# Performance work log

Hardware: AMD Instinct MI355X
Metric: run time of the kernel (lower is better)

Reference implementation:

```python
import jax, jax.numpy as jnp
import numpy as np
from jax import lax

T = 8192; BLK = 32; M = 64; C = 32; D = 512; HH = 256; L = 6; TEMP = 1.0

def _gru(x, Wih, Whh, bih, bhh, reverse=False):
    # x: (S, B, in) -> (S, B, h); PyTorch GRU cell math
    h0 = jnp.zeros((x.shape[1], Whh.shape[0]), x.dtype)
    xs = x[::-1] if reverse else x
    gi = xs @ Wih + bih
    def step(h, g):
        gh = h @ Whh + bhh
        ir, iz, inn = jnp.split(g, 3, -1)
        hr, hz, hn = jnp.split(gh, 3, -1)
        r = jax.nn.sigmoid(ir + hr)
        z = jax.nn.sigmoid(iz + hz)
        n = jnp.tanh(inn + r * hn)
        h = (1.0 - z) * n + z * h
        return h, h
    _, hs = lax.scan(step, h0, gi)
    return hs[::-1] if reverse else hs

def _xattn(X, Y, Xpos, Ypos, Wq, Wk, Wv, Wo, bo):
    # Y queries X; single head with head_dim = D (X2Y_map)
    q = (Y + Ypos) @ Wq
    k = (X + Xpos) @ Wk
    v = X @ Wv
    logits = jnp.einsum('ybd,xbd->byx', q, k) / jnp.sqrt(jnp.float32(q.shape[-1]))
    attn = jax.nn.softmax(logits, -1)
    out = jnp.einsum('byx,xbd->ybd', attn, v) @ Wo + bo
    return out, attn, logits

def _conv1(x, W, b, dil=1):
    y = lax.conv_general_dilated(x, W, (1,), 'SAME', rhs_dilation=(dil,), dimension_numbers=('NCH', 'OIH', 'NCH'))
    return y + b[None, :, None]

def _sim(x, W, b, text):
    v = x @ W + b
    v = v / jnp.linalg.norm(v, axis=-1, keepdims=True)
    t = text / jnp.linalg.norm(text, axis=-1, keepdims=True)
    return jnp.einsum('tbh,ch->tbc', v, t) / TEMP

def _segments(frame_feature, Wf2c, bf2c, text):
    # host-side argmax -> contiguous-run segmentation (mirrors utils.parse_label on CPU)
    sim = _sim(frame_feature, Wf2c, bf2c, text)
    pred = np.asarray(jnp.argmax(sim[:, 0], -1))
    change = np.concatenate([[0], (np.diff(pred) != 0).astype(np.int64)])
    seg_id = np.cumsum(change)
    S = int(seg_id[-1]) + 1
    starts = np.concatenate([[0], np.flatnonzero(change)])
    ends = np.concatenate([starts[1:] - 1, [len(pred) - 1]])
    centers = (starts + ends) // 2
    return jnp.asarray(seg_id), S, jnp.asarray(centers)

def _core(p, seg_id, S, centers):
    ff = p['frame_feature']
    cnt = jax.ops.segment_sum(jnp.ones((T,), jnp.float32), seg_id, S)
    seg = jax.ops.segment_sum(ff, seg_id, S) / cnt[:, None, None]  # frame->seg mean pool
    hf = _gru(seg, p['sg_Wih_f'], p['sg_Whh_f'], p['sg_bih_f'], p['sg_bhh_f'])
    hb = _gru(seg, p['sg_Wih_b'], p['sg_Whh_b'], p['sg_bih_b'], p['sg_bhh_b'], reverse=True)
    seg = jax.nn.relu(jnp.concatenate([hf, hb], -1)) @ p['Wcomb'] + p['bcomb']
    seg_pos = p['frame_pos'][centers]
    af, _, _ = _xattn(seg, p['action_feature'], seg_pos, p['action_pos'], p['f2a_Wq'], p['f2a_Wk'], p['f2a_Wv'], p['f2a_Wo'], p['f2a_bo'])
    af = _gru(af, p['ag_Wih'], p['ag_Whh'], p['ag_bih'], p['ag_bhh'])  # action branch GRU
    seg2, _, _ = _xattn(af, seg, p['action_pos'], seg_pos, p['a2f_Wq'], p['a2f_Wk'], p['a2f_Wv'], p['a2f_Wo'], p['a2f_bo'])
    s2f = seg2[seg_id]  # seg->frame upsample
    ff2 = jax.nn.relu(jnp.concatenate([s2f, ff], -1) @ p['Wsf'] + p['bsf'])
    x = jnp.transpose(ff2[:, 0])[None]  # (1, D, T)
    x = _conv1(x, p['tcn_in_W'], p['tcn_in_b'])
    for i in range(L):  # dilated residual TCN (MSTCN)
        y = jax.nn.relu(_conv1(x, p['tcn_dW'][i], p['tcn_db'][i], dil=2 ** i))
        x = x + _conv1(y, p['tcn_pW'][i], p['tcn_pb'][i])
    x = _conv1(x, p['tcn_out_W'], p['tcn_out_b'])
    ff_out = jnp.transpose(x[0])[:, None, :]
    return ff_out, af, seg2

def setup_inputs():
    ks = iter(jax.random.split(jax.random.key(0), 80))
    def rn(*shape):
        return jax.random.normal(next(ks), shape, dtype=jnp.float32)
    def z(n):
        return jnp.zeros((n,), jnp.float32)
    s = 0.05
    base = rn(T // BLK, 1, D)
    frame_feature = jnp.repeat(base, BLK, axis=0) + 0.01 * rn(T, 1, D)
    return {
        'frame_feature': frame_feature,
        'action_feature': rn(M, 1, D),
        'frame_pos': 0.02 * rn(T, 1, D),
        'action_pos': 0.02 * rn(M, 1, D),
        'text_emb': rn(C, 512),
        'Wf2c': s * rn(D, 512), 'bf2c': z(512),
        'Wa2c': s * rn(D, 512), 'ba2c': z(512),
        'Ws2c': s * rn(D, 512), 'bs2c': z(512),
        'sg_Wih_f': s * rn(D, 3 * HH), 'sg_Whh_f': s * rn(HH, 3 * HH), 'sg_bih_f': z(3 * HH), 'sg_bhh_f': z(3 * HH),
        'sg_Wih_b': s * rn(D, 3 * HH), 'sg_Whh_b': s * rn(HH, 3 * HH), 'sg_bih_b': z(3 * HH), 'sg_bhh_b': z(3 * HH),
        'Wcomb': s * rn(D, D), 'bcomb': z(D),
        'f2a_Wq': s * rn(D, D), 'f2a_Wk': s * rn(D, D), 'f2a_Wv': s * rn(D, D), 'f2a_Wo': s * rn(D, D), 'f2a_bo': z(D),
        'ag_Wih': s * rn(D, 3 * D), 'ag_Whh': s * rn(D, 3 * D), 'ag_bih': z(3 * D), 'ag_bhh': z(3 * D),
        'a2f_Wq': s * rn(D, D), 'a2f_Wk': s * rn(D, D), 'a2f_Wv': s * rn(D, D), 'a2f_Wo': s * rn(D, D), 'a2f_bo': z(D),
        'Wsf': s * rn(2 * D, D), 'bsf': z(D),
        'tcn_in_W': s * rn(D, D, 1), 'tcn_in_b': z(D),
        'tcn_dW': s * rn(L, D, D, 3), 'tcn_db': jnp.zeros((L, D), jnp.float32),
        'tcn_pW': s * rn(L, D, D, 1), 'tcn_pb': jnp.zeros((L, D), jnp.float32),
        'tcn_out_W': s * rn(D, D, 1), 'tcn_out_b': z(D),
    }

def reference(frame_feature, action_feature, frame_pos, action_pos, text_emb, Wf2c, bf2c, Wa2c, ba2c, Ws2c, bs2c, sg_Wih_f, sg_Whh_f, sg_bih_f, sg_bhh_f, sg_Wih_b, sg_Whh_b, sg_bih_b, sg_bhh_b, Wcomb, bcomb, f2a_Wq, f2a_Wk, f2a_Wv, f2a_Wo, f2a_bo, ag_Wih, ag_Whh, ag_bih, ag_bhh, a2f_Wq, a2f_Wk, a2f_Wv, a2f_Wo, a2f_bo, Wsf, bsf, tcn_in_W, tcn_in_b, tcn_dW, tcn_db, tcn_pW, tcn_pb, tcn_out_W, tcn_out_b):
    p = dict(locals())
    seg_id, S, centers = _segments(frame_feature, Wf2c, bf2c, text_emb)
    ff_out, af, seg2 = _core(p, seg_id, S, centers)
    frame_sim = _sim(ff_out, Wf2c, bf2c, text_emb)
    action_sim = _sim(af, Wa2c, ba2c, text_emb)
    seg_sim = _sim(seg2, Ws2c, bs2c, text_emb)
    return ff_out, af, frame_sim, action_sim, seg_sim
```

## Files before the change

kernel.cpp:

```cpp
#include <hip/hip_runtime.h>
#include <cstdint>
#include <cstddef>

__device__ __forceinline__ float sigf(float x) { return 1.f / (1.f + expf(-x)); }

__device__ __forceinline__ unsigned packh(float a, float b) {
  union { unsigned u; _Float16 h[2]; } cv;
  cv.h[0] = (_Float16)a; cv.h[1] = (_Float16)b; return cv.u;
}
__device__ __forceinline__ float2 uph(unsigned u) {
  union { unsigned uu; _Float16 h[2]; } cv; cv.uu = u;
  return make_float2((float)cv.h[0], (float)cv.h[1]);
}

typedef _Float16 f16x8 __attribute__((ext_vector_type(8)));
typedef float f32x16 __attribute__((ext_vector_type(16)));

static constexpr int TT = 8192;
static constexpr int MM = 64;
static constexpr int CC = 32;
static constexpr int DD = 512;
static constexpr unsigned GUARD_MAX = 1u << 30;

__global__ void zero_k(float* __restrict__ p, long n) {
  long i = (long)blockIdx.x * 256 + threadIdx.x;
  long stride = (long)gridDim.x * 256;
  for (; i < n; i += stride) p[i] = 0.f;
}

__global__ void copy_k(const float* __restrict__ a, float* __restrict__ o, int n) {
  int i = blockIdx.x * 256 + threadIdx.x;
  if (i < n) o[i] = a[i];
}
__global__ void addff_k(const float* __restrict__ a, const float* __restrict__ b, float* __restrict__ o, int n) {
  int i = blockIdx.x * 256 + threadIdx.x;
  if (i < n) o[i] = a[i] + b[i];
}
__global__ void acomb_k(const float* __restrict__ hf, const float* __restrict__ hb, float* __restrict__ o, int n) {
  int i = blockIdx.x * 256 + threadIdx.x;
  if (i >= n) return;
  int s = i >> 9, j = i & 511;
  float v = (j < 256) ? hf[(size_t)s * 256 + j] : hb[(size_t)s * 256 + (j - 256)];
  o[i] = fmaxf(v, 0.f);
}
__global__ void gatherpos_k(const float* __restrict__ fpos, const int* __restrict__ centers,
                            float* __restrict__ segpos, int n) {
  int i = blockIdx.x * 256 + threadIdx.x;
  if (i >= n) return;
  int s = i >> 9, dd = i & 511;
  int ct = centers[s];
  ct = ct < 0 ? 0 : (ct > TT - 1 ? TT - 1 : ct);
  segpos[i] = fpos[(size_t)ct * 512 + dd];
}

__global__ void tnorm_k(const float* __restrict__ text, float* __restrict__ tnorm) {
  int c = blockIdx.x * 256 + threadIdx.x;
  if (c >= 32) return;
  float s = 0.f;
  for (int dd = 0; dd < 512; dd++) { float v = text[(size_t)c * 512 + dd]; s += v * v; }
  tnorm[c] = sqrtf(s);
}

__global__ void prepM_k(const float* __restrict__ W, const float* __restrict__ b,
                        const float* __restrict__ text, const float* __restrict__ tnorm,
                        float* __restrict__ M, float* __restrict__ bdot) {
  int idx = blockIdx.x * 256 + threadIdx.x;
  if (idx < 512 * 32) {
    int k = idx >> 5, c = idx & 31;
    const float* wr = W + (size_t)k * 512;
    const float* tr = text + (size_t)c * 512;
    float s = 0.f;
    for (int dd = 0; dd < 512; dd++) s += wr[dd] * tr[dd];
    M[idx] = s / tnorm[c];
  }
  if (idx < 32) {
    const float* tr = text + (size_t)idx * 512;
    float s = 0.f;
    for (int dd = 0; dd < 512; dd++) s += b[dd] * tr[dd];
    bdot[idx] = s / tnorm[idx];
  }
}

__launch_bounds__(256)
__global__ void fargmax_k(const float* __restrict__ ff, const float* __restrict__ M,
                          const float* __restrict__ bdot, int* __restrict__ pred) {
  const int r = blockIdx.x * 8 + (threadIdx.x >> 5);
  const int c = threadIdx.x & 31;
  const float* fr = ff + (size_t)r * 512;
  float acc = bdot[c];
  for (int k = 0; k < 512; k++) acc += fr[k] * M[k * 32 + c];
  float best = acc; int bidx = c;
  for (int off = 16; off >= 1; off >>= 1) {
    const float ov = __shfl_xor(best, off);
    const int oi = __shfl_xor(bidx, off);
    if (ov > best || (ov == best && oi < bidx)) { best = ov; bidx = oi; }
  }
  if (c == 0) pred[r] = bidx;
}

__global__ void nlogit_k(const float* __restrict__ Q, const float* __restrict__ Kk,
                         float* __restrict__ L, int NY, int NX) {
  int idx = blockIdx.x * 256 + threadIdx.x;
  if (idx >= NY * NX) return;
  int y = idx / NX, x = idx - y * NX;
  const float* qr = Q + (size_t)y * 512;
  const float* kr = Kk + (size_t)x * 512;
  float d = 0.f;
  for (int k = 0; k < 512; k++) d += qr[k] * kr[k];
  L[idx] = d * 0.044194173824159216f;
}
__global__ void nsoft_k(float* __restrict__ L, int NY, int NX) {
  int y = blockIdx.x * 256 + threadIdx.x;
  if (y >= NY) return;
  float* row = L + (size_t)y * NX;
  float m = row[0];
  for (int x = 1; x < NX; x++) m = fmaxf(m, row[x]);
  float s = 0.f;
  for (int x = 0; x < NX; x++) { float p = expf(row[x] - m); row[x] = p; s += p; }
  const float inv = 1.f / s;
  for (int x = 0; x < NX; x++) row[x] *= inv;
}
__global__ void nav_k(const float* __restrict__ P, const float* __restrict__ V,
                      float* __restrict__ O, int NY, int NX) {
  int idx = blockIdx.x * 256 + threadIdx.x;
  if (idx >= NY * 512) return;
  int y = idx >> 9, dd = idx & 511;
  const float* pr = P + (size_t)y * NX;
  float o = 0.f;
  for (int x = 0; x < NX; x++) o += pr[x] * V[(size_t)x * 512 + dd];
  O[idx] = o;
}

__global__ void segscan_k(const int* __restrict__ pred, int* __restrict__ segid,
                          int* __restrict__ starts, int* __restrict__ centers,
                          int* __restrict__ cnts) {
  __shared__ int base[256];
  __shared__ int SS;
  const int tid = threadIdx.x;
  int lc = 0;
  unsigned flags = 0;
  int prev = (tid > 0) ? pred[tid * 32 - 1] : 0;
  for (int i = 0; i < 32; i++) {
    const int t = tid * 32 + i;
    const int cur = pred[t];
    const int c = (t > 0) && (cur != prev);
    prev = cur;
    flags |= ((unsigned)c) << i;
    lc += c;
  }
  base[tid] = lc;
  __syncthreads();
  if (tid == 0) {
    int run = 0;
    for (int i = 0; i < 256; i++) { const int v = base[i]; base[i] = run; run += v; }
    SS = run + 1;
  }
  __syncthreads();
  int b = base[tid];
  for (int i = 0; i < 32; i++) {
    const int t = tid * 32 + i;
    if ((flags >> i) & 1u) { b++; starts[b] = t; }
    segid[t] = b;
  }
  if (tid == 0) starts[0] = 0;
  __threadfence_block();
  __syncthreads();
  const int S = SS;
  for (int s = tid; s < TT; s += 256) {
    if (s < S) {
      const int e = (s == S - 1) ? (TT - 1) : (starts[s + 1] - 1);
      centers[s] = (starts[s] + e) >> 1;
      cnts[s] = e - starts[s] + 1;
    } else {
      starts[s] = 0; cnts[s] = 1; centers[s] = 0;
    }
  }
}

__global__ void segmean_k(const float* __restrict__ ff, const int* __restrict__ starts,
                          const int* __restrict__ cnts, float* __restrict__ segmean, int S) {
  int idx = blockIdx.x * 256 + threadIdx.x;
  if (idx >= S * 512) return;
  int s = idx >> 9, dd = idx & 511;
  int st = starts[s], n = cnts[s];
  st = st < 0 ? 0 : (st > TT - 1 ? TT - 1 : st);
  n = n < 1 ? 1 : n;
  if (st + n > TT) n = TT - st;
  float a = 0.f;
  for (int t = st; t < st + n; t++) a += ff[(size_t)t * 512 + dd];
  segmean[idx] = a / (float)n;
}

__launch_bounds__(192)
__global__ void gru_seg_mb_k(const float* __restrict__ gi_f, const float* __restrict__ gi_b,
                             const float* __restrict__ Whh_f, const float* __restrict__ bhh_f,
                             const float* __restrict__ Whh_b, const float* __restrict__ bhh_b,
                             float* __restrict__ hf, float* __restrict__ hb, int S,
                             int* __restrict__ flag_f, int* __restrict__ flag_b) {
  const int dir = blockIdx.x >> 2;
  const int part = blockIdx.x & 3;
  const float* gi = dir ? gi_b : gi_f;
  const float* Whh = dir ? Whh_b : Whh_f;
  const float* bhh = dir ? bhh_b : bhh_f;
  float* ho = dir ? hb : hf;
  int* flg = dir ? flag_b : flag_f;
  const int tid = threadIdx.x;
  const int h0 = part * 64;
  const int grp = tid >> 6;
  const int jj = tid & 63;
  const int j = grp * 256 + h0 + jj;
  __shared__ __align__(16) unsigned wlds[128 * 192];
  __shared__ __align__(16) unsigned hpk[128];
  __shared__ float hcur[256];
  __shared__ float rbuf[64], zbuf[64], gnbuf[64];
  for (int e = tid; e < 128 * 192; e += 192) {
    const int q = e / 768, rem = e % 768;
    const int g = rem >> 2, r = rem & 3;
    const int i2 = q * 4 + r;
    const int gg = (g >> 6) * 256 + h0 + (g & 63);
    wlds[e] = packh(Whh[(size_t)(2 * i2) * 768 + gg], Whh[(size_t)(2 * i2 + 1) * 768 + gg]);
  }
  for (int e = tid; e < 128; e += 192) hpk[e] = 0u;
  for (int e = tid; e < 256; e += 192) hcur[e] = 0.f;
  const float bj = bhh[j];
  __syncthreads();
  const uint4* hp4 = reinterpret_cast<const uint4*>(hpk);
  const uint4* wp4 = reinterpret_cast<const uint4*>(wlds);
  int s = dir ? (S - 1) : 0;
  float g_j = gi[(size_t)s * 768 + j];
  float g_n = (tid < 64) ? gi[(size_t)s * 768 + 512 + h0 + tid] : 0.f;
  for (int step = 0; step < S; step++) {
    float a0 = 0.f, a1 = 0.f, a2 = 0.f, a3 = 0.f;
#pragma unroll 8
    for (int q = 0; q < 32; q++) {
      const uint4 h4 = hp4[q];
      const uint4 w4 = wp4[q * 192 + tid];
      const float2 hh0 = uph(h4.x), hh1 = uph(h4.y), hh2 = uph(h4.z), hh3 = uph(h4.w);
      const float2 ww0 = uph(w4.x), ww1 = uph(w4.y), ww2 = uph(w4.z), ww3 = uph(w4.w);
      a0 += hh0.x * ww0.x + hh0.y * ww0.y;
      a1 += hh1.x * ww1.x + hh1.y * ww1.y;
      a2 += hh2.x * ww2.x + hh2.y * ww2.y;
      a3 += hh3.x * ww3.x + hh3.y * ww3.y;
    }
    const float gh = bj + (a0 + a1) + (a2 + a3);
    if (grp == 0)      rbuf[jj] = sigf(g_j + gh);
    else if (grp == 1) zbuf[jj] = sigf(g_j + gh);
    else               gnbuf[jj] = gh;
    __syncthreads();
    if (tid < 64) {
      const float nval = tanhf(g_n + rbuf[tid] * gnbuf[tid]);
      const float hn = (1.f - zbuf[tid]) * nval + zbuf[tid] * hcur[h0 + tid];
      __hip_atomic_store(&ho[(size_t)s * 256 + h0 + tid], hn,
                         __ATOMIC_RELAXED, __HIP_MEMORY_SCOPE_AGENT);
    }
    __syncthreads();
    if (tid == 0)
      __hip_atomic_store(&flg[step * 64 + part * 16], 1,
                         __ATOMIC_RELEASE, __HIP_MEMORY_SCOPE_AGENT);
    const int sn = dir ? (s - 1) : (s + 1);
    if (step + 1 < S) {
      g_j = gi[(size_t)sn * 768 + j];
      if (tid < 64) g_n = gi[(size_t)sn * 768 + 512 + h0 + tid];
    }
    if (tid < 4) {
      int* fp = &flg[step * 64 + tid * 16];
      unsigned guard = 0;
      while (__hip_atomic_load(fp, __ATOMIC_RELAXED, __HIP_MEMORY_SCOPE_AGENT) == 0 &&
             ++guard < GUARD_MAX) {
        __builtin_amdgcn_s_sleep(2);
      }
      (void)__hip_atomic_load(fp, __ATOMIC_ACQUIRE, __HIP_MEMORY_SCOPE_AGENT);
    }
    __syncthreads();
    for (int e = tid; e < 256; e += 192)
      hcur[e] = __hip_atomic_load(&ho[(size_t)s * 256 + e],
                                  __ATOMIC_RELAXED, __HIP_MEMORY_SCOPE_AGENT);
    __syncthreads();
    for (int e = tid; e < 128; e += 192) hpk[e] = packh(hcur[2 * e], hcur[2 * e + 1]);
    __syncthreads();
    s = sn;
  }
}

__launch_bounds__(128)
__global__ void gru_act_mb_k(const float* __restrict__ gi, const float* __restrict__ Whh,
                             const float* __restrict__ bhh, float* __restrict__ hout,
                             int steps, int* __restrict__ flg) {
  const int part = blockIdx.x;
  const int tid = threadIdx.x;
  const int h0 = part * 32;
  const int grp = tid >> 5;
  const int jj = tid & 31;
  const bool act = (tid < 96);
  const int j = act ? (grp * 512 + h0 + jj) : 0;
  __shared__ __align__(16) unsigned wlds[256 * 96];
  __shared__ __align__(16) unsigned hpk[256];
  __shared__ float hcur[512];
  __shared__ float rbuf[32], zbuf[32], gnbuf[32];
  for (int e = tid; e < 256 * 96; e += 128) {
    const int q = e / 384, rem = e % 384;
    const int g = rem >> 2, r = rem & 3;
    const int i2 = q * 4 + r;
    const int gg = (g >> 5) * 512 + h0 + (g & 31);
    wlds[e] = packh(Whh[(size_t)(2 * i2) * 1536 + gg], Whh[(size_t)(2 * i2 + 1) * 1536 + gg]);
  }
  for (int e = tid; e < 256; e += 128) hpk[e] = 0u;
  for (int e = tid; e < 512; e += 128) hcur[e] = 0.f;
  const float bj = act ? bhh[j] : 0.f;
  __syncthreads();
  const uint4* hp4 = reinterpret_cast<const uint4*>(hpk);
  const uint4* wp4 = reinterpret_cast<const uint4*>(wlds);
  float g_j = act ? gi[j] : 0.f;
  float g_n = (tid < 32) ? gi[1024 + h0 + tid] : 0.f;
  for (int step = 0; step < steps; step++) {
    if (act) {
      float a0 = 0.f, a1 = 0.f, a2 = 0.f, a3 = 0.f;
#pragma unroll 8
      for (int q = 0; q < 64; q++) {
        const uint4 h4 = hp4[q];
        const uint4 w4 = wp4[q * 96 + tid];
        const float2 hh0 = uph(h4.x), hh1 = uph(h4.y), hh2 = uph(h4.z), hh3 = uph(h4.w);
        const float2 ww0 = uph(w4.x), ww1 = uph(w4.y), ww2 = uph(w4.z), ww3 = uph(w4.w);
        a0 += hh0.x * ww0.x + hh0.y * ww0.y;
        a1 += hh1.x * ww1.x + hh1.y * ww1.y;
        a2 += hh2.x * ww2.x + hh2.y * ww2.y;
        a3 += hh3.x * ww3.x + hh3.y * ww3.y;
      }
      const float gh = bj + (a0 + a1) + (a2 + a3);
      if (grp == 0)      rbuf[jj] = sigf(g_j + gh);
      else if (grp == 1) zbuf[jj] = sigf(g_j + gh);
      else               gnbuf[jj] = gh;
    }
    __syncthreads();
    if (tid < 32) {
      const float nval = tanhf(g_n + rbuf[tid] * gnbuf[tid]);
      const float hn = (1.f - zbuf[tid]) * nval + zbuf[tid] * hcur[h0 + tid];
      __hip_atomic_store(&hout[(size_t)step * 512 + h0 + tid], hn,
                         __ATOMIC_RELAXED, __HIP_MEMORY_SCOPE_AGENT);
    }
    __syncthreads();
    if (tid == 0)
      __hip_atomic_store(&flg[step * 256 + part * 16], 1,
                         __ATOMIC_RELEASE, __HIP_MEMORY_SCOPE_AGENT);
    if (step + 1 < steps) {
      if (act) g_j = gi[(size_t)(step + 1) * 1536 + j];
      if (tid < 32) g_n = gi[(size_t)(step + 1) * 1536 + 1024 + h0 + tid];
    }
    if (tid < 16) {
      int* fp = &flg[step * 256 + tid * 16];
      unsigned guard = 0;
      while (__hip_atomic_load(fp, __ATOMIC_RELAXED, __HIP_MEMORY_SCOPE_AGENT) == 0 &&
             ++guard < GUARD_MAX) {
        __builtin_amdgcn_s_sleep(2);
      }
      (void)__hip_atomic_load(fp, __ATOMIC_ACQUIRE, __HIP_MEMORY_SCOPE_AGENT);
    }
    __syncthreads();
    for (int e = tid; e < 512; e += 128)
      hcur[e] = __hip_atomic_load(&hout[(size_t)step * 512 + e],
                                  __ATOMIC_RELAXED, __HIP_MEMORY_SCOPE_AGENT);
    __syncthreads();
    for (int e = tid; e < 256; e += 128) hpk[e] = packh(hcur[2 * e], hcur[2 * e + 1]);
    __syncthreads();
  }
}

__launch_bounds__(256)
__global__ void gemmm_k(const float* __restrict__ A, const float* __restrict__ B,
                        const float* __restrict__ bias, float* __restrict__ C,
                        int M, int N, int K) {
  __shared__ __align__(16) _Float16 As16[64][72];
  __shared__ __align__(16) _Float16 Bs16[128][72];
  const int n0 = blockIdx.x * 128, m0 = blockIdx.y * 64;
  const int tid = threadIdx.x;
  const int l = tid & 63, w = tid >> 6;
  const int wm = w & 1, wn = w >> 1;
  const int l31 = l & 31, q = l >> 5;
  f32x16 acc0, acc1;
#pragma unroll
  for (int i = 0; i < 16; i++) { acc0[i] = 0.f; acc1[i] = 0.f; }
  const int am = tid >> 2, ak0 = (tid & 3) * 16;
  const int bk = tid >> 2, bn0 = (tid & 3) * 32;
  for (int kc = 0; kc < K; kc += 64) {
    __syncthreads();
#pragma unroll
    for (int kk = 0; kk < 16; kk += 4) {
      const float4 av = *reinterpret_cast<const float4*>(A + (size_t)(m0 + am) * K + kc + ak0 + kk);
      As16[am][ak0 + kk + 0] = (_Float16)av.x; As16[am][ak0 + kk + 1] = (_Float16)av.y;
      As16[am][ak0 + kk + 2] = (_Float16)av.z; As16[am][ak0 + kk + 3] = (_Float16)av.w;
    }
#pragma unroll
    for (int nn = 0; nn < 32; nn += 4) {
      const float4 bv = *reinterpret_cast<const float4*>(B + (size_t)(kc + bk) * N + n0 + bn0 + nn);
      Bs16[bn0 + nn + 0][bk] = (_Float16)bv.x; Bs16[bn0 + nn + 1][bk] = (_Float16)bv.y;
      Bs16[bn0 + nn + 2][bk] = (_Float16)bv.z; Bs16[bn0 + nn + 3][bk] = (_Float16)bv.w;
    }
    __syncthreads();
#pragma unroll
    for (int ks = 0; ks < 4; ks++) {
      const int k0 = ks * 16 + q * 8;
      const f16x8 a = *reinterpret_cast<const f16x8*>(&As16[wm * 32 + l31][k0]);
      const f16x8 b0 = *reinterpret_cast<const f16x8*>(&Bs16[wn * 64 + l31][k0]);
      acc0 = __builtin_amdgcn_mfma_f32_32x32x16_f16(a, b0, acc0, 0, 0, 0);
      const f16x8 b1 = *reinterpret_cast<const f16x8*>(&Bs16[wn * 64 + 32 + l31][k0]);
      acc1 = __builtin_amdgcn_mfma_f32_32x32x16_f16(a, b1, acc1, 0, 0, 0);
    }
  }
#pragma unroll
  for (int r = 0; r < 16; r++) {
    const int m = m0 + wm * 32 + (r & 3) + 8 * (r >> 2) + 4 * q;
    {
      const int n = n0 + wn * 64 + l31;
      float v = acc0[r];
      if (bias) v += bias[n];
      C[(size_t)m * N + n] = v;
    }
    {
      const int n = n0 + wn * 64 + 32 + l31;
      float v = acc1[r];
      if (bias) v += bias[n];
      C[(size_t)m * N + n] = v;
    }
  }
}

__launch_bounds__(256)
__global__ void ff2m_k(const float* __restrict__ seg2, const float* __restrict__ ff,
                       const int* __restrict__ segid, const float* __restrict__ Wsf,
                       const float* __restrict__ bsf, float* __restrict__ Y, int S) {
  __shared__ __align__(16) _Float16 As16[64][72];
  __shared__ __align__(16) _Float16 Bs16[128][72];
  const int t0 = blockIdx.x * 128, nd0 = blockIdx.y * 64;
  const int tid = threadIdx.x;
  const int l = tid & 63, w = tid >> 6;
  const int wm = w & 1, wn = w >> 1;
  const int l31 = l & 31, q = l >> 5;
  f32x16 acc0, acc1;
#pragma unroll
  for (int i = 0; i < 16; i++) { acc0[i] = 0.f; acc1[i] = 0.f; }
  const int ak = tid >> 2, an0 = (tid & 3) * 16;
  const int bt = tid >> 1, bk0 = (tid & 1) * 32;
  const int tglob = t0 + bt;
  int sid = segid[tglob];
  sid = sid < 0 ? 0 : (sid >= S ? S - 1 : sid);
  for (int kc = 0; kc < 1024; kc += 64) {
    __syncthreads();
#pragma unroll
    for (int nn = 0; nn < 16; nn += 4) {
      const float4 wv = *reinterpret_cast<const float4*>(Wsf + (size_t)(kc + ak) * 512 + nd0 + an0 + nn);
      As16[an0 + nn + 0][ak] = (_Float16)wv.x; As16[an0 + nn + 1][ak] = (_Float16)wv.y;
      As16[an0 + nn + 2][ak] = (_Float16)wv.z; As16[an0 + nn + 3][ak] = (_Float16)wv.w;
    }
    {
      const float* src = (kc < 512) ? (seg2 + (size_t)sid * 512 + kc + bk0)
                                    : (ff + (size_t)tglob * 512 + (kc - 512) + bk0);
#pragma unroll
      for (int kk = 0; kk < 32; kk += 4) {
        const float4 xv = *reinterpret_cast<const float4*>(src + kk);
        Bs16[bt][bk0 + kk + 0] = (_Float16)xv.x; Bs16[bt][bk0 + kk + 1] = (_Float16)xv.y;
        Bs16[bt][bk0 + kk + 2] = (_Float16)xv.z; Bs16[bt][bk0 + kk + 3] = (_Float16)xv.w;
      }
    }
    __syncthreads();
#pragma unroll
    for (int ks = 0; ks < 4; ks++) {
      const int k0 = ks * 16 + q * 8;
      const f16x8 a = *reinterpret_cast<const f16x8*>(&As16[wm * 32 + l31][k0]);
      const f16x8 b0 = *reinterpret_cast<const f16x8*>(&Bs16[wn * 64 + l31][k0]);
      acc0 = __builtin_amdgcn_mfma_f32_32x32x16_f16(a, b0, acc0, 0, 0, 0);
      const f16x8 b1 = *reinterpret_cast<const f16x8*>(&Bs16[wn * 64 + 32 + l31][k0]);
      acc1 = __builtin_amdgcn_mfma_f32_32x32x16_f16(a, b1, acc1, 0, 0, 0);
    }
  }
#pragma unroll
  for (int r = 0; r < 16; r++) {
    const int nd = nd0 + wm * 32 + (r & 3) + 8 * (r >> 2) + 4 * q;
    const float bb = bsf[nd];
    {
      const int t = t0 + wn * 64 + l31;
      Y[(size_t)nd * TT + t] = fmaxf(acc0[r] + bb, 0.f);
    }
    {
      const int t = t0 + wn * 64 + 32 + l31;
      Y[(size_t)nd * TT + t] = fmaxf(acc1[r] + bb, 0.f);
    }
  }
}

template<int NTAPS, int RELU, int RES>
__launch_bounds__(256)
__global__ void convm_k(const float* __restrict__ X, const float* __restrict__ W,
                        const float* __restrict__ bias, const float* __restrict__ Res,
                        float* __restrict__ Y, int dil) {
  const int d = (NTAPS == 3) ? dil : 0;
  const int width = 128 + 2 * d;
  __shared__ __align__(16) _Float16 Ws16[NTAPS][64][72];
  __shared__ __align__(16) _Float16 Xs16[192][72];
  const int t0 = blockIdx.x * 128, c0 = blockIdx.y * 64;
  const int tid = threadIdx.x;
  const int l = tid & 63, w = tid >> 6;
  const int wm = w & 1, wn = w >> 1;
  const int l31 = l & 31, q = l >> 5;
  f32x16 acc0, acc1;
#pragma unroll
  for (int i = 0; i < 16; i++) { acc0[i] = 0.f; acc1[i] = 0.f; }
  const int xk = tid >> 2;
  const int xu0 = tid & 3;
  for (int kc = 0; kc < 512; kc += 64) {
    __syncthreads();
    {
      const float* xr = X + (size_t)(kc + xk) * TT;
      for (int u = xu0; u < width; u += 4) {
        const int gt = t0 - d + u;
        const float v = (gt >= 0 && gt < TT) ? xr[gt] : 0.f;
        Xs16[u][xk] = (_Float16)v;
      }
    }
    if (NTAPS == 3) {
      for (int e = tid; e < 64 * 48; e += 256) {
        const int c = e / 48;
        const int f0 = (e - c * 48) * 4;
        const float4 wv = *reinterpret_cast<const float4*>(
            W + (size_t)(c0 + c) * 1536 + (size_t)kc * 3 + f0);
        const float vv[4] = {wv.x, wv.y, wv.z, wv.w};
#pragma unroll
        for (int t = 0; t < 4; t++) {
          const int f = f0 + t;
          Ws16[f % 3][c][f / 3] = (_Float16)vv[t];
        }
      }
    } else {
      for (int e = tid; e < 1024; e += 256) {
        const int c = e >> 4, i0 = (e & 15) << 2;
        const float4 wv = *reinterpret_cast<const float4*>(W + (size_t)(c0 + c) * 512 + kc + i0);
        Ws16[0][c][i0 + 0] = (_Float16)wv.x; Ws16[0][c][i0 + 1] = (_Float16)wv.y;
        Ws16[0][c][i0 + 2] = (_Float16)wv.z; Ws16[0][c][i0 + 3] = (_Float16)wv.w;
      }
    }
    __syncthreads();
#pragma unroll
    for (int tap = 0; tap < NTAPS; tap++) {
#pragma unroll
      for (int ks = 0; ks < 4; ks++) {
        const int k0 = ks * 16 + q * 8;
        const f16x8 a = *reinterpret_cast<const f16x8*>(&Ws16[tap][wm * 32 + l31][k0]);
        const int row0 = wn * 64 + l31 + tap * d;
        const f16x8 b0 = *reinterpret_cast<const f16x8*>(&Xs16[row0][k0]);
        acc0 = __builtin_amdgcn_mfma_f32_32x32x16_f16(a, b0, acc0, 0, 0, 0);
        const f16x8 b1 = *reinterpret_cast<const f16x8*>(&Xs16[row0 + 32][k0]);
        acc1 = __builtin_amdgcn_mfma_f32_32x32x16_f16(a, b1, acc1, 0, 0, 0);
      }
    }
  }
#pragma unroll
  for (int r = 0; r < 16; r++) {
    const int m = wm * 32 + (r & 3) + 8 * (r >> 2) + 4 * q;
    const int c = c0 + m;
    const float bb = bias[c];
    {
      const int t = t0 + wn * 64 + l31;
      float v = acc0[r] + bb;
      if (RES) v += Res[(size_t)c * TT + t];
      if (RELU) v = fmaxf(v, 0.f);
      Y[(size_t)c * TT + t] = v;
    }
    {
      const int t = t0 + wn * 64 + 32 + l31;
      float v = acc1[r] + bb;
      if (RES) v += Res[(size_t)c * TT + t];
      if (RELU) v = fmaxf(v, 0.f);
      Y[(size_t)c * TT + t] = v;
    }
  }
}

__launch_bounds__(256)
__global__ void temit_k(const float* __restrict__ Xin, float* __restrict__ outp,
                        float* __restrict__ Aout) {
  __shared__ float tile[32][33];
  const int t0 = blockIdx.x * 32, d0 = blockIdx.y * 32;
  const int lx = threadIdx.x & 31, ly = threadIdx.x >> 5;
#pragma unroll
  for (int r = 0; r < 4; r++)
    tile[ly + 8 * r][lx] = Xin[(size_t)(d0 + ly + 8 * r) * TT + t0 + lx];
  __syncthreads();
#pragma unroll
  for (int r = 0; r < 4; r++) {
    const int t = t0 + ly + 8 * r, dd = d0 + lx;
    const float v = tile[lx][ly + 8 * r];
    outp[(size_t)t * 512 + dd] = v;
    Aout[(size_t)t * 512 + dd] = v;
  }
}

__launch_bounds__(256)
__global__ void csim_k(const float* __restrict__ V, const float* __restrict__ text,
                       const float* __restrict__ tnorm, float* __restrict__ out) {
  __shared__ float vs[512];
  __shared__ float red[4];
  const int r = blockIdx.x, tid = threadIdx.x;
  const float a = V[(size_t)r * 512 + tid];
  const float b = V[(size_t)r * 512 + 256 + tid];
  vs[tid] = a; vs[tid + 256] = b;
  float ssp = a * a + b * b;
  for (int off = 32; off >= 1; off >>= 1) ssp += __shfl_xor(ssp, off);
  if ((tid & 63) == 0) red[tid >> 6] = ssp;
  __syncthreads();
  const float ss = red[0] + red[1] + red[2] + red[3];
  const int c = tid >> 3, p = tid & 7;
  const float* tr = text + (size_t)c * 512 + p * 64;
  const float* vr = vs + p * 64;
  float d = 0.f;
#pragma unroll
  for (int k = 0; k < 64; k++) d += vr[k] * tr[k];
  for (int off = 4; off >= 1; off >>= 1) d += __shfl_xor(d, off);
  if (p == 0) out[(size_t)r * 32 + c] = d / (sqrtf(ss) * tnorm[c]);
}

extern "C" void kernel_launch(void* const* d_in, const int* in_sizes, int n_in,
                              void* d_out, int out_size, void* d_ws, size_t ws_size,
                              hipStream_t stream) {
  const float* in_ff   = (const float*)d_in[0];
  const float* in_act  = (const float*)d_in[1];
  const float* in_fpos = (const float*)d_in[2];
  const float* in_apos = (const float*)d_in[3];
  const float* in_text = (const float*)d_in[4];
  const float* Wf2c = (const float*)d_in[5];  const float* bf2c = (const float*)d_in[6];
  const float* Wa2c = (const float*)d_in[7];  const float* ba2c = (const float*)d_in[8];
  const float* Ws2c = (const float*)d_in[9];  const float* bs2c = (const float*)d_in[10];
  const float* Wih_f = (const float*)d_in[11]; const float* Whh_f = (const float*)d_in[12];
  const float* bih_f = (const float*)d_in[13]; const float* bhh_f = (const float*)d_in[14];
  const float* Wih_b = (const float*)d_in[15]; const float* Whh_b = (const float*)d_in[16];
  const float* bih_b = (const float*)d_in[17]; const float* bhh_b = (const float*)d_in[18];
  const float* Wcomb = (const float*)d_in[19]; const float* bcomb = (const float*)d_in[20];
  const float* f2a_Wq = (const float*)d_in[21]; const float* f2a_Wk = (const float*)d_in[22];
  const float* f2a_Wv = (const float*)d_in[23]; const float* f2a_Wo = (const float*)d_in[24];
  const float* f2a_bo = (const float*)d_in[25];
  const float* ag_Wih = (const float*)d_in[26]; const float* ag_Whh = (const float*)d_in[27];
  const float* ag_bih = (const float*)d_in[28]; const float* ag_bhh = (const float*)d_in[29];
  const float* a2f_Wq = (const float*)d_in[30]; const float* a2f_Wk = (const float*)d_in[31];
  const float* a2f_Wv = (const float*)d_in[32]; const float* a2f_Wo = (const float*)d_in[33];
  const float* a2f_bo = (const float*)d_in[34];
  const float* Wsf = (const float*)d_in[35]; const float* bsf = (const float*)d_in[36];
  const float* tcn_inW = (const float*)d_in[37]; const float* tcn_inb = (const float*)d_in[38];
  const float* tcn_dW = (const float*)d_in[39]; const float* tcn_db = (const float*)d_in[40];
  const float* tcn_pW = (const float*)d_in[41]; const float* tcn_pb = (const float*)d_in[42];
  const float* tcn_outW = (const float*)d_in[43]; const float* tcn_outb = (const float*)d_in[44];

  int S = (out_size - (TT * DD + MM * DD + TT * CC + MM * CC)) / CC;
  if (S < 1) S = 1;
  if (S > TT) S = TT;
  const int Spad = (S + 63) & ~63;

  char* ws = (char*)d_ws;
  size_t off = 0;
  auto alloc = [&](size_t b) -> char* { char* p = ws + off; off += (b + 255) & ~(size_t)255; return p; };
  int* flgF = (int*)alloc((size_t)S * 64 * 4);
  int* flgB = (int*)alloc((size_t)S * 64 * 4);
  int* flgA = (int*)alloc((size_t)MM * 256 * 4);
  const size_t zero_words = off / 4;
  float* Mmat = (float*)alloc((size_t)512 * 32 * 4);
  float* bdot = (float*)alloc(32 * 4);
  const size_t BTD = (size_t)TT * DD * 4;
  float* bufA = (float*)alloc(BTD);
  float* bufB = (float*)alloc(BTD);
  int* pred    = (int*)alloc((size_t)TT * 4);
  int* segid   = (int*)alloc((size_t)TT * 4);
  int* starts  = (int*)alloc((size_t)TT * 4);
  int* centers = (int*)alloc((size_t)TT * 4);
  int* cnts    = (int*)alloc((size_t)TT * 4);
  float* tnorm = (float*)alloc(32 * 4);
  float* segmean = (float*)alloc((size_t)Spad * 512 * 4);
  float* gif  = (float*)alloc((size_t)Spad * 768 * 4);
  float* gib  = (float*)alloc((size_t)Spad * 768 * 4);
  float* hfb  = (float*)alloc((size_t)Spad * 256 * 4);
  float* hbb  = (float*)alloc((size_t)Spad * 256 * 4);
  float* acmb = (float*)alloc((size_t)Spad * 512 * 4);
  float* segc = (float*)alloc((size_t)Spad * 512 * 4);
  float* segpos = (float*)alloc((size_t)Spad * 512 * 4);
  float* kin  = (float*)alloc((size_t)Spad * 512 * 4);
  float* kf2a = (float*)alloc((size_t)Spad * 512 * 4);
  float* vf2a = (float*)alloc((size_t)Spad * 512 * 4);
  float* q2   = (float*)alloc((size_t)Spad * 512 * 4);
  float* att2 = (float*)alloc((size_t)Spad * 512 * 4);
  float* seg2 = (float*)alloc((size_t)Spad * 512 * 4);
  float* vseg = (float*)alloc((size_t)Spad * 512 * 4);
  float* pbuf = (float*)alloc((size_t)64 * Spad * 4);
  float* qin  = (float*)alloc((size_t)64 * 512 * 4);
  float* qf2a = (float*)alloc((size_t)64 * 512 * 4);
  float* att1 = (float*)alloc((size_t)64 * 512 * 4);
  float* af0  = (float*)alloc((size_t)64 * 512 * 4);
  float* aggi = (float*)alloc((size_t)64 * 1536 * 4);
  float* afg  = (float*)alloc((size_t)64 * 512 * 4);
  float* k2in = (float*)alloc((size_t)64 * 512 * 4);
  float* k2   = (float*)alloc((size_t)64 * 512 * 4);
  float* v2   = (float*)alloc((size_t)64 * 512 * 4);
  float* vaf  = (float*)alloc((size_t)64 * 512 * 4);
  (void)ws_size; (void)in_sizes; (void)n_in;

  float* outp = (float*)d_out;
  float* out_ff   = outp;
  float* out_af   = outp + (size_t)TT * DD;
  float* out_fsim = out_af + (size_t)MM * DD;
  float* out_asim = out_fsim + (size_t)TT * CC;
  float* out_ssim = out_asim + (size_t)MM * CC;

  auto GR = [](long n) { return (unsigned)((n + 255) / 256); };
  const unsigned Sg = (unsigned)(Spad / 64);

  zero_k<<<256, 256, 0, stream>>>((float*)d_ws, (long)zero_words);

  tnorm_k<<<1, 256, 0, stream>>>(in_text, tnorm);

  prepM_k<<<64, 256, 0, stream>>>(Wf2c, bf2c, in_text, tnorm, Mmat, bdot);
  fargmax_k<<<TT / 8, 256, 0, stream>>>(in_ff, Mmat, bdot, pred);
  segscan_k<<<1, 256, 0, stream>>>(pred, segid, starts, centers, cnts);
  segmean_k<<<GR((long)S * 512), 256, 0, stream>>>(in_ff, starts, cnts, segmean, S);

  gemmm_k<<<dim3(6, Sg), 256, 0, stream>>>(segmean, Wih_f, bih_f, gif, Spad, 768, 512);
  gemmm_k<<<dim3(6, Sg), 256, 0, stream>>>(segmean, Wih_b, bih_b, gib, Spad, 768, 512);
  gru_seg_mb_k<<<8, 192, 0, stream>>>(gif, gib, Whh_f, bhh_f, Whh_b, bhh_b,
                                      hfb, hbb, S, flgF, flgB);
  acomb_k<<<GR((long)S * 512), 256, 0, stream>>>(hfb, hbb, acmb, S * 512);
  gemmm_k<<<dim3(4, Sg), 256, 0, stream>>>(acmb, Wcomb, bcomb, segc, Spad, 512, 512);
  gatherpos_k<<<GR((long)S * 512), 256, 0, stream>>>(in_fpos, centers, segpos, S * 512);

  addff_k<<<GR(64 * 512), 256, 0, stream>>>(in_act, in_apos, qin, 64 * 512);
  addff_k<<<GR((long)S * 512), 256, 0, stream>>>(segc, segpos, kin, S * 512);
  gemmm_k<<<dim3(4, 1), 256, 0, stream>>>(qin, f2a_Wq, nullptr, qf2a, 64, 512, 512);
  gemmm_k<<<dim3(4, Sg), 256, 0, stream>>>(kin, f2a_Wk, nullptr, kf2a, Spad, 512, 512);
  gemmm_k<<<dim3(4, Sg), 256, 0, stream>>>(segc, f2a_Wv, nullptr, vf2a, Spad, 512, 512);
  nlogit_k<<<GR((long)64 * S), 256, 0, stream>>>(qf2a, kf2a, pbuf, 64, S);
  nsoft_k<<<1, 256, 0, stream>>>(pbuf, 64, S);
  nav_k<<<GR(64 * 512), 256, 0, stream>>>(pbuf, vf2a, att1, 64, S);
  gemmm_k<<<dim3(4, 1), 256, 0, stream>>>(att1, f2a_Wo, f2a_bo, af0, 64, 512, 512);

  gemmm_k<<<dim3(12, 1), 256, 0, stream>>>(af0, ag_Wih, ag_bih, aggi, 64, 1536, 512);
  gru_act_mb_k<<<16, 128, 0, stream>>>(aggi, ag_Whh, ag_bhh, afg, MM, flgA);
  copy_k<<<GR(64 * 512), 256, 0, stream>>>(afg, out_af, 64 * 512);

  addff_k<<<GR(64 * 512), 256, 0, stream>>>(afg, in_apos, k2in, 64 * 512);
  gemmm_k<<<dim3(4, Sg), 256, 0, stream>>>(kin, a2f_Wq, nullptr, q2, Spad, 512, 512);
  gemmm_k<<<dim3(4, 1), 256, 0, stream>>>(k2in, a2f_Wk, nullptr, k2, 64, 512, 512);
  gemmm_k<<<dim3(4, 1), 256, 0, stream>>>(afg, a2f_Wv, nullptr, v2, 64, 512, 512);
  nlogit_k<<<GR((long)S * 64), 256, 0, stream>>>(q2, k2, pbuf, S, 64);
  nsoft_k<<<GR(S), 256, 0, stream>>>(pbuf, S, 64);
  nav_k<<<GR((long)S * 512), 256, 0, stream>>>(pbuf, v2, att2, S, 64);
  gemmm_k<<<dim3(4, Sg), 256, 0, stream>>>(att2, a2f_Wo, a2f_bo, seg2, Spad, 512, 512);

  ff2m_k<<<dim3(64, 8), 256, 0, stream>>>(seg2, in_ff, segid, Wsf, bsf, bufA, S);
  convm_k<1, 0, 0><<<dim3(64, 8), 256, 0, stream>>>(bufA, tcn_inW, tcn_inb, nullptr, bufB, 1);
  for (int l = 0; l < 6; l++) {
    convm_k<3, 1, 0><<<dim3(64, 8), 256, 0, stream>>>(
        bufB, tcn_dW + (size_t)l * 512 * 512 * 3, tcn_db + (size_t)l * 512, nullptr, bufA, 1 << l);
    convm_k<1, 0, 1><<<dim3(64, 8), 256, 0, stream>>>(
        bufA, tcn_pW + (size_t)l * 512 * 512, tcn_pb + (size_t)l * 512, bufB, bufB, 1);
  }
  convm_k<1, 0, 0><<<dim3(64, 8), 256, 0, stream>>>(bufB, tcn_outW, tcn_outb, nullptr, bufA, 1);
  temit_k<<<dim3(256, 16), 256, 0, stream>>>(bufA, out_ff, bufB);

  gemmm_k<<<dim3(4, 128), 256, 0, stream>>>(bufB, Wf2c, bf2c, bufA, TT, 512, 512);
  csim_k<<<TT, 256, 0, stream>>>(bufA, in_text, tnorm, out_fsim);
  gemmm_k<<<dim3(4, 1), 256, 0, stream>>>(afg, Wa2c, ba2c, vaf, 64, 512, 512);
  csim_k<<<64, 256, 0, stream>>>(vaf, in_text, tnorm, out_asim);
  gemmm_k<<<dim3(4, Sg), 256, 0, stream>>>(seg2, Ws2c, bs2c, vseg, Spad, 512, 512);
  csim_k<<<(unsigned)S, 256, 0, stream>>>(vseg, in_text, tnorm, out_ssim);
}
```

Measured before the change: 4.246 ms.

## Replace flag-based GRU cross-block sync with NaN-sentinel polling on hidden state

The multi-block GRU kernels no longer publish and poll separate per-step flags. The hidden-state buffers are prefilled with quiet NaN, and each thread polls its own element until it is no longer NaN. This removes one barrier, the release-store/acquire round trip and the flag buffer zeroing from each recurrent step, which should shorten the serial latency per step. It depends on relaxed stores being seen as whole values, drops acquire ordering, and would hang up to the guard limit if a real hidden value were ever NaN.

Measured after the change: 3.965 ms. 1.07x faster.

```diff
diff --git a/kernel.cpp b/kernel.cpp
--- a/kernel.cpp
+++ b/kernel.cpp
@@ -22,10 +22,11 @@
 static constexpr int DD = 512;
 static constexpr unsigned GUARD_MAX = 1u << 30;
 
-__global__ void zero_k(float* __restrict__ p, long n) {
+__global__ void nanfill_k(float* __restrict__ p, long n) {
   long i = (long)blockIdx.x * 256 + threadIdx.x;
   long stride = (long)gridDim.x * 256;
-  for (; i < n; i += stride) p[i] = 0.f;
+  const float qnan = __int_as_float(0x7fc00000);
+  for (; i < n; i += stride) p[i] = qnan;
 }
 
 __global__ void copy_k(const float* __restrict__ a, float* __restrict__ o, int n) {
@@ -195,15 +196,13 @@
 __global__ void gru_seg_mb_k(const float* __restrict__ gi_f, const float* __restrict__ gi_b,
                              const float* __restrict__ Whh_f, const float* __restrict__ bhh_f,
                              const float* __restrict__ Whh_b, const float* __restrict__ bhh_b,
-                             float* __restrict__ hf, float* __restrict__ hb, int S,
-                             int* __restrict__ flag_f, int* __restrict__ flag_b) {
+                             float* __restrict__ hf, float* __restrict__ hb, int S) {
   const int dir = blockIdx.x >> 2;
   const int part = blockIdx.x & 3;
   const float* gi = dir ? gi_b : gi_f;
   const float* Whh = dir ? Whh_b : Whh_f;
   const float* bhh = dir ? bhh_b : bhh_f;
   float* ho = dir ? hb : hf;
-  int* flg = dir ? flag_b : flag_f;
   const int tid = threadIdx.x;
   const int h0 = part * 64;
   const int grp = tid >> 6;
@@ -253,28 +252,23 @@
       __hip_atomic_store(&ho[(size_t)s * 256 + h0 + tid], hn,
                          __ATOMIC_RELAXED, __HIP_MEMORY_SCOPE_AGENT);
     }
-    __syncthreads();
-    if (tid == 0)
-      __hip_atomic_store(&flg[step * 64 + part * 16], 1,
-                         __ATOMIC_RELEASE, __HIP_MEMORY_SCOPE_AGENT);
     const int sn = dir ? (s - 1) : (s + 1);
     if (step + 1 < S) {
       g_j = gi[(size_t)sn * 768 + j];
       if (tid < 64) g_n = gi[(size_t)sn * 768 + 512 + h0 + tid];
     }
-    if (tid < 4) {
-      int* fp = &flg[step * 64 + tid * 16];
+    __syncthreads();
+    for (int e = tid; e < 256; e += 192) {
+      float v = __hip_atomic_load(&ho[(size_t)s * 256 + e],
+                                  __ATOMIC_RELAXED, __HIP_MEMORY_SCOPE_AGENT);
       unsigned guard = 0;
-      while (__hip_atomic_load(fp, __ATOMIC_RELAXED, __HIP_MEMORY_SCOPE_AGENT) == 0 &&
-             ++guard < GUARD_MAX) {
-        __builtin_amdgcn_s_sleep(2);
+      while (v != v && ++guard < GUARD_MAX) {
+        __builtin_amdgcn_s_sleep(1);
+        v = __hip_atomic_load(&ho[(size_t)s * 256 + e],
+                              __ATOMIC_RELAXED, __HIP_MEMORY_SCOPE_AGENT);
       }
-      (void)__hip_atomic_load(fp, __ATOMIC_ACQUIRE, __HIP_MEMORY_SCOPE_AGENT);
-    }
-    __syncthreads();
-    for (int e = tid; e < 256; e += 192)
-      hcur[e] = __hip_atomic_load(&ho[(size_t)s * 256 + e],
-                                  __ATOMIC_RELAXED, __HIP_MEMORY_SCOPE_AGENT);
+      hcur[e] = v;
+    }
     __syncthreads();
     for (int e = tid; e < 128; e += 192) hpk[e] = packh(hcur[2 * e], hcur[2 * e + 1]);
     __syncthreads();
@@ -285,7 +279,7 @@
 __launch_bounds__(128)
 __global__ void gru_act_mb_k(const float* __restrict__ gi, const float* __restrict__ Whh,
                              const float* __restrict__ bhh, float* __restrict__ hout,
-                             int steps, int* __restrict__ flg) {
+                             int steps) {
   const int part = blockIdx.x;
   const int tid = threadIdx.x;
   const int h0 = part * 32;
@@ -338,27 +332,22 @@
       __hip_atomic_store(&hout[(size_t)step * 512 + h0 + tid], hn,
                          __ATOMIC_RELAXED, __HIP_MEMORY_SCOPE_AGENT);
     }
-    __syncthreads();
-    if (tid == 0)
-      __hip_atomic_store(&flg[step * 256 + part * 16], 1,
-                         __ATOMIC_RELEASE, __HIP_MEMORY_SCOPE_AGENT);
     if (step + 1 < steps) {
       if (act) g_j = gi[(size_t)(step + 1) * 1536 + j];
       if (tid < 32) g_n = gi[(size_t)(step + 1) * 1536 + 1024 + h0 + tid];
     }
-    if (tid < 16) {
-      int* fp = &flg[step * 256 + tid * 16];
+    __syncthreads();
+    for (int e = tid; e < 512; e += 128) {
+      float v = __hip_atomic_load(&hout[(size_t)step * 512 + e],
+                                  __ATOMIC_RELAXED, __HIP_MEMORY_SCOPE_AGENT);
       unsigned guard = 0;
-      while (__hip_atomic_load(fp, __ATOMIC_RELAXED, __HIP_MEMORY_SCOPE_AGENT) == 0 &&
-             ++guard < GUARD_MAX) {
-        __builtin_amdgcn_s_sleep(2);
+      while (v != v && ++guard < GUARD_MAX) {
+        __builtin_amdgcn_s_sleep(1);
+        v = __hip_atomic_load(&hout[(size_t)step * 512 + e],
+                              __ATOMIC_RELAXED, __HIP_MEMORY_SCOPE_AGENT);
       }
-      (void)__hip_atomic_load(fp, __ATOMIC_ACQUIRE, __HIP_MEMORY_SCOPE_AGENT);
-    }
-    __syncthreads();
-    for (int e = tid; e < 512; e += 128)
-      hcur[e] = __hip_atomic_load(&hout[(size_t)step * 512 + e],
-                                  __ATOMIC_RELAXED, __HIP_MEMORY_SCOPE_AGENT);
+      hcur[e] = v;
+    }
     __syncthreads();
     for (int e = tid; e < 256; e += 128) hpk[e] = packh(hcur[2 * e], hcur[2 * e + 1]);
     __syncthreads();
@@ -655,10 +644,6 @@
   char* ws = (char*)d_ws;
   size_t off = 0;
   auto alloc = [&](size_t b) -> char* { char* p = ws + off; off += (b + 255) & ~(size_t)255; return p; };
-  int* flgF = (int*)alloc((size_t)S * 64 * 4);
-  int* flgB = (int*)alloc((size_t)S * 64 * 4);
-  int* flgA = (int*)alloc((size_t)MM * 256 * 4);
-  const size_t zero_words = off / 4;
   float* Mmat = (float*)alloc((size_t)512 * 32 * 4);
   float* bdot = (float*)alloc(32 * 4);
   const size_t BTD = (size_t)TT * DD * 4;
@@ -708,9 +693,11 @@
   auto GR = [](long n) { return (unsigned)((n + 255) / 256); };
   const unsigned Sg = (unsigned)(Spad / 64);
 
-  zero_k<<<256, 256, 0, stream>>>((float*)d_ws, (long)zero_words);
-
   tnorm_k<<<1, 256, 0, stream>>>(in_text, tnorm);
+
+  nanfill_k<<<128, 256, 0, stream>>>(hfb, (long)Spad * 256);
+  nanfill_k<<<128, 256, 0, stream>>>(hbb, (long)Spad * 256);
+  nanfill_k<<<32, 256, 0, stream>>>(afg, (long)64 * 512);
 
   prepM_k<<<64, 256, 0, stream>>>(Wf2c, bf2c, in_text, tnorm, Mmat, bdot);
   fargmax_k<<<TT / 8, 256, 0, stream>>>(in_ff, Mmat, bdot, pred);
@@ -719,8 +706,7 @@
 
   gemmm_k<<<dim3(6, Sg), 256, 0, stream>>>(segmean, Wih_f, bih_f, gif, Spad, 768, 512);
   gemmm_k<<<dim3(6, Sg), 256, 0, stream>>>(segmean, Wih_b, bih_b, gib, Spad, 768, 512);
-  gru_seg_mb_k<<<8, 192, 0, stream>>>(gif, gib, Whh_f, bhh_f, Whh_b, bhh_b,
-                                      hfb, hbb, S, flgF, flgB);
+  gru_seg_mb_k<<<8, 192, 0, stream>>>(gif, gib, Whh_f, bhh_f, Whh_b, bhh_b, hfb, hbb, S);
   acomb_k<<<GR((long)S * 512), 256, 0, stream>>>(hfb, hbb, acmb, S * 512);
   gemmm_k<<<dim3(4, Sg), 256, 0, stream>>>(acmb, Wcomb, bcomb, segc, Spad, 512, 512);
   gatherpos_k<<<GR((long)S * 512), 256, 0, stream>>>(in_fpos, centers, segpos, S * 512);
@@ -736,7 +722,7 @@
   gemmm_k<<<dim3(4, 1), 256, 0, stream>>>(att1, f2a_Wo, f2a_bo, af0, 64, 512, 512);
 
   gemmm_k<<<dim3(12, 1), 256, 0, stream>>>(af0, ag_Wih, ag_bih, aggi, 64, 1536, 512);
-  gru_act_mb_k<<<16, 128, 0, stream>>>(aggi, ag_Whh, ag_bhh, afg, MM, flgA);
+  gru_act_mb_k<<<16, 128, 0, stream>>>(aggi, ag_Whh, ag_bhh, afg, MM);
   copy_k<<<GR(64 * 512), 256, 0, stream>>>(afg, out_af, 64 * 512);
 
   addff_k<<<GR(64 * 512), 256, 0, stream>>>(afg, in_apos, k2in, 64 * 512);
```
